# Optimization experiments

Hardware: AMD Instinct MI355X
Metric: run time of the kernel (lower is better)

Reference implementation:

```python
import jax, jax.numpy as jnp
import numpy as np

N_NODES = 100000


def gcn_conv(x, edge_index, W, b, n_nodes):
    """PyG GCNConv: linear -> add self-loops -> symmetric-normalized scatter-sum -> bias."""
    h = x @ W  # [N, F_out]
    loop = jnp.arange(n_nodes, dtype=edge_index.dtype)
    src = jnp.concatenate([edge_index[0], loop])
    dst = jnp.concatenate([edge_index[1], loop])
    # degree of destination nodes (self-loops included)
    deg = jax.ops.segment_sum(jnp.ones_like(dst, dtype=h.dtype), dst, num_segments=n_nodes)
    dinv = jnp.where(deg > 0, jax.lax.rsqrt(deg), 0.0)
    norm = dinv[src] * dinv[dst]  # [E+N]
    msg = h[src] * norm[:, None]  # gather + scale
    out = jax.ops.segment_sum(msg, dst, num_segments=n_nodes)  # scatter-add
    return out + b


def setup_inputs() -> dict:
    key = jax.random.key(0)
    k1, k2, k3, k4 = jax.random.split(key, 4)
    d_in, hidden, out = 128, 256, 64
    x = jax.random.normal(k1, (N_NODES, d_in), dtype=jnp.float32)
    edge_index = jax.random.randint(k2, (2, 800000), 0, N_NODES, dtype=jnp.int64)
    W1 = jax.random.normal(k3, (d_in, hidden), dtype=jnp.float32) * (1.0 / np.sqrt(d_in))
    b1 = jnp.zeros((hidden,), dtype=jnp.float32)
    W2 = jax.random.normal(k4, (hidden, out), dtype=jnp.float32) * (1.0 / np.sqrt(hidden))
    b2 = jnp.zeros((out,), dtype=jnp.float32)
    return {"x": x, "edge_index": edge_index, "W1": W1, "b1": b1, "W2": W2, "b2": b2}


def reference(x, edge_index, W1, b1, W2, b2):
    h = jax.nn.relu(gcn_conv(x, edge_index, W1, b1, N_NODES))
    # dropout p=0 (module default) -> identity
    return gcn_conv(h, edge_index, W2, b2, N_NODES)
```

## Files before the change

kernel.cpp:

```cpp
#include <hip/hip_runtime.h>
#include <hip/hip_bf16.h>

#define N_NODES 100000
#define D_IN 128
#define HID 256
#define D_OUT 64
#define TR 32
#define NBUK 196
#define BSH 9

typedef __attribute__((ext_vector_type(8))) short bf8;
typedef __attribute__((ext_vector_type(4))) float f4;

static __device__ __forceinline__ unsigned short f2bf(float f) {
    __hip_bfloat16 h = __float2bfloat16(f);
    return *reinterpret_cast<unsigned short*>(&h);
}
static __device__ __forceinline__ float bflo(unsigned int u) { return __uint_as_float(u << 16); }
static __device__ __forceinline__ float bfhi(unsigned int u) { return __uint_as_float(u & 0xffff0000u); }

static __device__ __forceinline__ void fma8(float* a, float w, uint4 u) {
    a[0] += w * bflo(u.x); a[1] += w * bfhi(u.x);
    a[2] += w * bflo(u.y); a[3] += w * bfhi(u.y);
    a[4] += w * bflo(u.z); a[5] += w * bfhi(u.z);
    a[6] += w * bflo(u.w); a[7] += w * bfhi(u.w);
}
static __device__ __forceinline__ void fma4(float* a, float w, uint2 u) {
    a[0] += w * bflo(u.x); a[1] += w * bfhi(u.x);
    a[2] += w * bflo(u.y); a[3] += w * bfhi(u.y);
}


__global__ __launch_bounds__(256) void k_prep(const float* __restrict__ x,
                                              unsigned long long* __restrict__ xb,
                                              const float* __restrict__ W1,
                                              unsigned short* __restrict__ W1t,
                                              const float* __restrict__ W2,
                                              unsigned short* __restrict__ W2t,
                                              int* __restrict__ bhist) {
    int b = blockIdx.x, t = threadIdx.x;
    if (b < 12500) {
        int i = b * 256 + t;
        float4 v = ((const float4*)x)[i];
        unsigned long long o = (unsigned long long)f2bf(v.x) |
                               ((unsigned long long)f2bf(v.y) << 16) |
                               ((unsigned long long)f2bf(v.z) << 32) |
                               ((unsigned long long)f2bf(v.w) << 48);
        xb[i] = o;
    } else if (b < 12628) {
        int i = (b - 12500) * 256 + t;
        int n = i >> 7, k = i & 127;
        W1t[i] = f2bf(W1[k * HID + n]);
    } else if (b < 12692) {
        int i = (b - 12628) * 256 + t;
        int n = i >> 8, k = i & 255;
        W2t[i] = f2bf(W2[k * D_OUT + n]);
    } else {
        if (t < NBUK) bhist[t] = 0;
    }
}


__global__ __launch_bounds__(256) void k_hist(const int* __restrict__ dst, int E,
                                              int* __restrict__ bhist) {
    __shared__ int h[NBUK];
    int t = threadIdx.x;
    if (t < NBUK) h[t] = 0;
    __syncthreads();
    int base = blockIdx.x * 4096;
    for (int j = 0; j < 16; j++) {
        int e = base + j * 256 + t;
        if (e < E) atomicAdd(&h[dst[e] >> BSH], 1);
    }
    __syncthreads();
    if (t < NBUK && h[t] > 0) atomicAdd(&bhist[t], h[t]);
}

__global__ __launch_bounds__(256) void k_scanB(const int* __restrict__ bhist,
                                               int* __restrict__ bbase,
                                               int* __restrict__ bcursor) {
    __shared__ int s[256];
    int t = threadIdx.x;
    int v = (t < NBUK) ? bhist[t] : 0;
    s[t] = v;
    __syncthreads();
    for (int off = 1; off < 256; off <<= 1) {
        int u = (t >= off) ? s[t - off] : 0;
        __syncthreads();
        s[t] += u;
        __syncthreads();
    }
    if (t < NBUK) {
        bbase[t] = s[t] - v;
        bcursor[t] = s[t] - v;
    }
    if (t == NBUK - 1) bbase[NBUK] = s[t];
}

__global__ __launch_bounds__(256) void k_bin(const int* __restrict__ src,
                                             const int* __restrict__ dst, int E,
                                             int* __restrict__ bcursor,
                                             unsigned int* __restrict__ bin) {
    __shared__ int histL[NBUK], baseL[NBUK], rankL[NBUK];
    int t = threadIdx.x;
    if (t < NBUK) {
        histL[t] = 0;
        rankL[t] = 0;
    }
    __syncthreads();
    int base = blockIdx.x * 4096;
    int ss[16], dd[16];
#pragma unroll
    for (int j = 0; j < 16; j++) {
        int e = base + j * 256 + t;
        if (e < E) {
            ss[j] = src[e];
            dd[j] = dst[e];
            atomicAdd(&histL[dd[j] >> BSH], 1);
        } else {
            dd[j] = -1;
        }
    }
    __syncthreads();
    if (t < NBUK && histL[t] > 0) baseL[t] = atomicAdd(&bcursor[t], histL[t]);
    __syncthreads();
#pragma unroll
    for (int j = 0; j < 16; j++) {
        if (dd[j] >= 0) {
            int bu = dd[j] >> BSH;
            int r = atomicAdd(&rankL[bu], 1);
            bin[baseL[bu] + r] = ((unsigned int)(dd[j] & 511) << 17) | (unsigned int)ss[j];
        }
    }
}

__global__ __launch_bounds__(256) void k_cnt(const unsigned int* __restrict__ bin,
                                             const int* __restrict__ bbase,
                                             int* __restrict__ cnt) {
    __shared__ int c[512];
    int b = blockIdx.x, t = threadIdx.x;
    c[t] = 0;
    c[t + 256] = 0;
    __syncthreads();
    int lo = bbase[b], hi = bbase[b + 1];
    for (int e = lo + t; e < hi; e += 256) atomicAdd(&c[bin[e] >> 17], 1);
    __syncthreads();
    int node0 = b << BSH;
    int nbn = N_NODES - node0;
    if (nbn > 512) nbn = 512;
    if (t < nbn) cnt[node0 + t] = c[t];
    if (t + 256 < nbn) cnt[node0 + t + 256] = c[t + 256];
}

__global__ __launch_bounds__(256) void k_scan_part(const int* __restrict__ cnt,
                                                   int* __restrict__ row_ptr,
                                                   int* __restrict__ bsum,
                                                   float* __restrict__ dinv, int n) {
    __shared__ int s[256];
    int t = threadIdx.x, i = blockIdx.x * 256 + t;
    int v = (i < n) ? cnt[i] : 0;
    s[t] = v;
    __syncthreads();
    for (int off = 1; off < 256; off <<= 1) {
        int u = (t >= off) ? s[t - off] : 0;
        __syncthreads();
        s[t] += u;
        __syncthreads();
    }
    if (i < n) {
        row_ptr[i] = s[t] - v;
        dinv[i] = rsqrtf((float)v + 1.0f);
    }
    if (t == 255) bsum[blockIdx.x] = s[255];
}

__global__ __launch_bounds__(512) void k_scan_base(int* __restrict__ bsum,
                                                   int* __restrict__ row_ptr, int nb, int n) {
    __shared__ int s[512];
    int t = threadIdx.x;
    int v = (t < nb) ? bsum[t] : 0;
    s[t] = v;
    __syncthreads();
    for (int off = 1; off < 512; off <<= 1) {
        int u = (t >= off) ? s[t - off] : 0;
        __syncthreads();
        s[t] += u;
        __syncthreads();
    }
    if (t < nb) bsum[t] = s[t] - v;
    if (t == 511) row_ptr[n] = s[511];
}

__global__ void k_scan_fin(int* __restrict__ row_ptr, const int* __restrict__ bsum, int n) {
    int i = blockIdx.x * blockDim.x + threadIdx.x;
    if (i < n) row_ptr[i] += bsum[i >> 8];
}

__global__ __launch_bounds__(256) void k_place(const unsigned int* __restrict__ bin,
                                               const int* __restrict__ bbase,
                                               const int* __restrict__ row_ptr,
                                               const float* __restrict__ dinv,
                                               int2* __restrict__ cw) {
    __shared__ int cur[512];
    __shared__ float dl[512];
    int b = blockIdx.x, t = threadIdx.x;
    int node0 = b << BSH;
    int nbn = N_NODES - node0;
    if (nbn > 512) nbn = 512;
    if (t < nbn) {
        cur[t] = row_ptr[node0 + t];
        dl[t] = dinv[node0 + t];
    }
    if (t + 256 < nbn) {
        cur[t + 256] = row_ptr[node0 + t + 256];
        dl[t + 256] = dinv[node0 + t + 256];
    }
    __syncthreads();
    int lo = bbase[b], hi = bbase[b + 1];
    for (int e = lo + t; e < hi; e += 256) {
        unsigned int rec = bin[e];
        int s = rec & 0x1FFFF;
        int dloc = rec >> 17;
        int pos = atomicAdd(&cur[dloc], 1);
        int2 v;
        v.x = s;
        v.y = __float_as_int(dinv[s] * dl[dloc]);
        cw[pos] = v;
    }
}


__global__ __launch_bounds__(256) void k_pull1(const int* __restrict__ row_ptr,
                                               const int2* __restrict__ cw,
                                               const uint4* __restrict__ xb4,
                                               const float* __restrict__ dinv,
                                               uint4* __restrict__ agg4) {
    int wave = (blockIdx.x * 256 + threadIdx.x) >> 6;
    int lane = threadIdx.x & 63;
    int g = lane >> 4, l = lane & 15;
    int node = wave * 4 + g;
    int beg = row_ptr[node], end = row_ptr[node + 1];
    float di = dinv[node];
    float a[8] = {0, 0, 0, 0, 0, 0, 0, 0};
    fma8(a, di * di, xb4[(size_t)node * 16 + l]);
    int e = beg;
    for (; e + 4 <= end; e += 4) {
        int2 c0 = cw[e + 0], c1 = cw[e + 1], c2 = cw[e + 2], c3 = cw[e + 3];
        uint4 u0 = xb4[(size_t)c0.x * 16 + l];
        uint4 u1 = xb4[(size_t)c1.x * 16 + l];
        uint4 u2 = xb4[(size_t)c2.x * 16 + l];
        uint4 u3 = xb4[(size_t)c3.x * 16 + l];
        fma8(a, __int_as_float(c0.y), u0);
        fma8(a, __int_as_float(c1.y), u1);
        fma8(a, __int_as_float(c2.y), u2);
        fma8(a, __int_as_float(c3.y), u3);
    }
    for (; e < end; e++) {
        int2 c = cw[e];
        fma8(a, __int_as_float(c.y), xb4[(size_t)c.x * 16 + l]);
    }
    uint4 o;
    o.x = (unsigned int)f2bf(a[0]) | ((unsigned int)f2bf(a[1]) << 16);
    o.y = (unsigned int)f2bf(a[2]) | ((unsigned int)f2bf(a[3]) << 16);
    o.z = (unsigned int)f2bf(a[4]) | ((unsigned int)f2bf(a[5]) << 16);
    o.w = (unsigned int)f2bf(a[6]) | ((unsigned int)f2bf(a[7]) << 16);
    agg4[(size_t)node * 16 + l] = o;
}


__global__ __launch_bounds__(256) void k_fused_mfma(unsigned short* __restrict__ agg,
                                                    const unsigned short* __restrict__ W1t,
                                                    const float* __restrict__ b1,
                                                    const unsigned short* __restrict__ W2t) {
    __shared__ char sA[TR * D_IN * 2];
    __shared__ char sH[TR * HID * 2];
    int t = threadIdx.x, wave = t >> 6, lane = t & 63;
    int lr = lane & 15, lg = lane >> 4;
    size_t row0 = (size_t)blockIdx.x * TR;

    {
        const float4* g = (const float4*)(agg + row0 * D_IN);
#pragma unroll
        for (int c0 = 0; c0 < 2; c0++) {
            int c = c0 * 256 + t;
            int row = c >> 4;
            *(float4*)(sA + ((c * 16) ^ ((row & 7) << 4))) = g[c];
        }
    }
    __syncthreads();

    f4 acc1[4][2];
#pragma unroll
    for (int tt = 0; tt < 4; tt++)
#pragma unroll
        for (int h = 0; h < 2; h++) acc1[tt][h] = (f4){0.f, 0.f, 0.f, 0.f};

#pragma unroll
    for (int kk = 0; kk < 4; kk++) {
        bf8 a0 = *(const bf8*)(sA + ((lr * 256 + kk * 64 + lg * 16) ^ ((lr & 7) << 4)));
        bf8 a1 = *(const bf8*)(sA + (((16 + lr) * 256 + kk * 64 + lg * 16) ^ (((16 + lr) & 7) << 4)));
#pragma unroll
        for (int tt = 0; tt < 4; tt++) {
            bf8 b = *(const bf8*)(W1t + (size_t)(wave * 64 + tt * 16 + lr) * D_IN + kk * 32 + lg * 8);
            acc1[tt][0] = __builtin_amdgcn_mfma_f32_16x16x32_bf16(a0, b, acc1[tt][0], 0, 0, 0);
            acc1[tt][1] = __builtin_amdgcn_mfma_f32_16x16x32_bf16(a1, b, acc1[tt][1], 0, 0, 0);
        }
    }

#pragma unroll
    for (int tt = 0; tt < 4; tt++) {
        int colc = wave * 64 + tt * 16 + lr;
        float bias = b1[colc];
#pragma unroll
        for (int h = 0; h < 2; h++) {
#pragma unroll
            for (int ri = 0; ri < 4; ri++) {
                int row = h * 16 + lg * 4 + ri;
                float hv = acc1[tt][h][ri] + bias;
                hv = hv > 0.f ? hv : 0.f;
                *(unsigned short*)(sH + ((row * 512 + colc * 2) ^ ((row & 7) << 4))) = f2bf(hv);
            }
        }
    }
    __syncthreads();

    f4 acc2[2];
    acc2[0] = (f4){0.f, 0.f, 0.f, 0.f};
    acc2[1] = (f4){0.f, 0.f, 0.f, 0.f};
#pragma unroll
    for (int kk = 0; kk < 8; kk++) {
        bf8 a0 = *(const bf8*)(sH + ((lr * 512 + kk * 64 + lg * 16) ^ ((lr & 7) << 4)));
        bf8 a1 = *(const bf8*)(sH + (((16 + lr) * 512 + kk * 64 + lg * 16) ^ (((16 + lr) & 7) << 4)));
        bf8 b = *(const bf8*)(W2t + (size_t)(wave * 16 + lr) * HID + kk * 32 + lg * 8);
        acc2[0] = __builtin_amdgcn_mfma_f32_16x16x32_bf16(a0, b, acc2[0], 0, 0, 0);
        acc2[1] = __builtin_amdgcn_mfma_f32_16x16x32_bf16(a1, b, acc2[1], 0, 0, 0);
    }
    int colc = wave * 16 + lr;
#pragma unroll
    for (int h = 0; h < 2; h++)
#pragma unroll
        for (int ri = 0; ri < 4; ri++) {
            int row = h * 16 + lg * 4 + ri;
            agg[(row0 + row) * 128 + colc] = f2bf(acc2[h][ri]);
        }
}


__global__ __launch_bounds__(256) void k_pull2(const int* __restrict__ row_ptr,
                                               const int2* __restrict__ cw,
                                               const uint2* __restrict__ m2,
                                               const float* __restrict__ dinv,
                                               const float* __restrict__ b2,
                                               float4* __restrict__ out4) {
    int wave = (blockIdx.x * 256 + threadIdx.x) >> 6;
    int lane = threadIdx.x & 63;
    int g = lane >> 4, l = lane & 15;
    int node = wave * 4 + g;
    int beg = row_ptr[node], end = row_ptr[node + 1];
    float di = dinv[node];
    float a[4] = {0, 0, 0, 0};
    fma4(a, di * di, m2[(size_t)node * 32 + l]);
    int e = beg;
    for (; e + 4 <= end; e += 4) {
        int2 c0 = cw[e + 0], c1 = cw[e + 1], c2 = cw[e + 2], c3 = cw[e + 3];
        uint2 u0 = m2[(size_t)c0.x * 32 + l];
        uint2 u1 = m2[(size_t)c1.x * 32 + l];
        uint2 u2 = m2[(size_t)c2.x * 32 + l];
        uint2 u3 = m2[(size_t)c3.x * 32 + l];
        fma4(a, __int_as_float(c0.y), u0);
        fma4(a, __int_as_float(c1.y), u1);
        fma4(a, __int_as_float(c2.y), u2);
        fma4(a, __int_as_float(c3.y), u3);
    }
    for (; e < end; e++) {
        int2 c = cw[e];
        fma4(a, __int_as_float(c.y), m2[(size_t)c.x * 32 + l]);
    }
    float4 bv = ((const float4*)b2)[l];
    float4 o;
    o.x = a[0] + bv.x;
    o.y = a[1] + bv.y;
    o.z = a[2] + bv.z;
    o.w = a[3] + bv.w;
    out4[(size_t)node * 16 + l] = o;
}


extern "C" void kernel_launch(void* const* d_in, const int* in_sizes, int n_in,
                              void* d_out, int out_size, void* d_ws, size_t ws_size,
                              hipStream_t stream) {
    const float* x  = (const float*)d_in[0];
    const int*   ei = (const int*)d_in[1];
    const float* W1 = (const float*)d_in[2];
    const float* b1 = (const float*)d_in[3];
    const float* W2 = (const float*)d_in[4];
    const float* b2 = (const float*)d_in[5];
    float* out = (float*)d_out;

    const int E = in_sizes[1] / 2;
    const int* src = ei;
    const int* dst = ei + E;

    char* ws = (char*)d_ws;
    int* cnt            = (int*)(ws + 0);
    int* bsum           = cnt + 100096;
    int* row_ptr        = (int*)(ws + 402176);
    int2* cw            = (int2*)(ws + 802560);
    float* dinv         = (float*)(ws + 7202560);
    unsigned short* W1t = (unsigned short*)(ws + 7602944);
    unsigned short* W2t = (unsigned short*)(ws + 7668480);
    unsigned short* xb  = (unsigned short*)(ws + 7701248);
    unsigned short* aggb = (unsigned short*)(ws + 33301248);
    int* bhist          = (int*)aggb;
    int* bbase          = bhist + 256;
    int* bcursor        = bhist + 512;
    unsigned int* bin   = (unsigned int*)((char*)aggb + 4096);

    const int NB = (N_NODES + 255) / 256;
    const int NBB = (E + 4095) / 4096;

    k_prep<<<12693, 256, 0, stream>>>(x, (unsigned long long*)xb, W1, W1t, W2, W2t, bhist);

    k_hist<<<NBB, 256, 0, stream>>>(dst, E, bhist);
    k_scanB<<<1, 256, 0, stream>>>(bhist, bbase, bcursor);
    k_bin<<<NBB, 256, 0, stream>>>(src, dst, E, bcursor, bin);
    k_cnt<<<NBUK, 256, 0, stream>>>(bin, bbase, cnt);
    k_scan_part<<<NB, 256, 0, stream>>>(cnt, row_ptr, bsum, dinv, N_NODES);
    k_scan_base<<<1, 512, 0, stream>>>(bsum, row_ptr, NB, N_NODES);
    k_scan_fin<<<NB, 256, 0, stream>>>(row_ptr, bsum, N_NODES);
    k_place<<<NBUK, 256, 0, stream>>>(bin, bbase, row_ptr, dinv, cw);

    k_pull1<<<6250, 256, 0, stream>>>(row_ptr, cw, (const uint4*)xb, dinv, (uint4*)aggb);

    k_fused_mfma<<<N_NODES / TR, 256, 0, stream>>>(aggb, W1t, b1, W2t);

    k_pull2<<<6250, 256, 0, stream>>>(row_ptr, cw, (const uint2*)aggb, dinv, b2, (float4*)out);
}
```

Measured before the change: 167.5 us.

## Make fused MFMA kernel persistent with register-resident weight fragments

The fused two-layer MFMA kernel now launches 625 blocks that each loop over five 32-row tiles, instead of one block per tile. The W1/W2 fragments and bias are loaded into registers once per block rather than once per tile. The A operand is read straight from global memory, dropping the shared-memory staging buffer and one barrier. The cost is much higher register pressure (about 96 VGPRs for weights alone), which may lower occupancy, and less parallelism to hide the uncoalesced global reads of A.

```diff
diff --git a/kernel.cpp b/kernel.cpp
--- a/kernel.cpp
+++ b/kernel.cpp
@@ -8,6 +8,7 @@
 #define TR 32
 #define NBUK 196
 #define BSH 9
+#define MGRID 625
 
 typedef __attribute__((ext_vector_type(8))) short bf8;
 typedef __attribute__((ext_vector_type(4))) float f4;
@@ -272,77 +273,80 @@
                                                     const unsigned short* __restrict__ W1t,
                                                     const float* __restrict__ b1,
                                                     const unsigned short* __restrict__ W2t) {
-    __shared__ char sA[TR * D_IN * 2];
     __shared__ char sH[TR * HID * 2];
     int t = threadIdx.x, wave = t >> 6, lane = t & 63;
     int lr = lane & 15, lg = lane >> 4;
-    size_t row0 = (size_t)blockIdx.x * TR;
-
-    {
-        const float4* g = (const float4*)(agg + row0 * D_IN);
-#pragma unroll
-        for (int c0 = 0; c0 < 2; c0++) {
-            int c = c0 * 256 + t;
-            int row = c >> 4;
-            *(float4*)(sA + ((c * 16) ^ ((row & 7) << 4))) = g[c];
+
+    bf8 w1f[4][4];
+#pragma unroll
+    for (int kk = 0; kk < 4; kk++)
+#pragma unroll
+        for (int tt = 0; tt < 4; tt++)
+            w1f[kk][tt] = *(const bf8*)(W1t + (size_t)(wave * 64 + tt * 16 + lr) * D_IN + kk * 32 + lg * 8);
+    bf8 w2f[8];
+#pragma unroll
+    for (int kk = 0; kk < 8; kk++)
+        w2f[kk] = *(const bf8*)(W2t + (size_t)(wave * 16 + lr) * HID + kk * 32 + lg * 8);
+    float bias[4];
+#pragma unroll
+    for (int tt = 0; tt < 4; tt++) bias[tt] = b1[wave * 64 + tt * 16 + lr];
+
+    for (int it = 0; it < 5; it++) {
+        size_t row0 = ((size_t)blockIdx.x + (size_t)it * MGRID) * TR;
+
+        f4 acc1[4][2];
+#pragma unroll
+        for (int tt = 0; tt < 4; tt++)
+#pragma unroll
+            for (int h = 0; h < 2; h++) acc1[tt][h] = (f4){0.f, 0.f, 0.f, 0.f};
+
+#pragma unroll
+        for (int kk = 0; kk < 4; kk++) {
+            bf8 a0 = *(const bf8*)(agg + (row0 + lr) * 128 + kk * 32 + lg * 8);
+            bf8 a1 = *(const bf8*)(agg + (row0 + 16 + lr) * 128 + kk * 32 + lg * 8);
+#pragma unroll
+            for (int tt = 0; tt < 4; tt++) {
+                acc1[tt][0] = __builtin_amdgcn_mfma_f32_16x16x32_bf16(a0, w1f[kk][tt], acc1[tt][0], 0, 0, 0);
+                acc1[tt][1] = __builtin_amdgcn_mfma_f32_16x16x32_bf16(a1, w1f[kk][tt], acc1[tt][1], 0, 0, 0);
+            }
         }
-    }
-    __syncthreads();
-
-    f4 acc1[4][2];
-#pragma unroll
-    for (int tt = 0; tt < 4; tt++)
-#pragma unroll
-        for (int h = 0; h < 2; h++) acc1[tt][h] = (f4){0.f, 0.f, 0.f, 0.f};
-
-#pragma unroll
-    for (int kk = 0; kk < 4; kk++) {
-        bf8 a0 = *(const bf8*)(sA + ((lr * 256 + kk * 64 + lg * 16) ^ ((lr & 7) << 4)));
-        bf8 a1 = *(const bf8*)(sA + (((16 + lr) * 256 + kk * 64 + lg * 16) ^ (((16 + lr) & 7) << 4)));
+
 #pragma unroll
         for (int tt = 0; tt < 4; tt++) {
-            bf8 b = *(const bf8*)(W1t + (size_t)(wave * 64 + tt * 16 + lr) * D_IN + kk * 32 + lg * 8);
-            acc1[tt][0] = __builtin_amdgcn_mfma_f32_16x16x32_bf16(a0, b, acc1[tt][0], 0, 0, 0);
-            acc1[tt][1] = __builtin_amdgcn_mfma_f32_16x16x32_bf16(a1, b, acc1[tt][1], 0, 0, 0);
+            int colc = wave * 64 + tt * 16 + lr;
+#pragma unroll
+            for (int h = 0; h < 2; h++) {
+#pragma unroll
+                for (int ri = 0; ri < 4; ri++) {
+                    int row = h * 16 + lg * 4 + ri;
+                    float hv = acc1[tt][h][ri] + bias[tt];
+                    hv = hv > 0.f ? hv : 0.f;
+                    *(unsigned short*)(sH + ((row * 512 + colc * 2) ^ ((row & 7) << 4))) = f2bf(hv);
+                }
+            }
         }
-    }
-
-#pragma unroll
-    for (int tt = 0; tt < 4; tt++) {
-        int colc = wave * 64 + tt * 16 + lr;
-        float bias = b1[colc];
-#pragma unroll
-        for (int h = 0; h < 2; h++) {
+        __syncthreads();
+
+        f4 acc2[2];
+        acc2[0] = (f4){0.f, 0.f, 0.f, 0.f};
+        acc2[1] = (f4){0.f, 0.f, 0.f, 0.f};
+#pragma unroll
+        for (int kk = 0; kk < 8; kk++) {
+            bf8 a0 = *(const bf8*)(sH + ((lr * 512 + kk * 64 + lg * 16) ^ ((lr & 7) << 4)));
+            bf8 a1 = *(const bf8*)(sH + (((16 + lr) * 512 + kk * 64 + lg * 16) ^ (((16 + lr) & 7) << 4)));
+            acc2[0] = __builtin_amdgcn_mfma_f32_16x16x32_bf16(a0, w2f[kk], acc2[0], 0, 0, 0);
+            acc2[1] = __builtin_amdgcn_mfma_f32_16x16x32_bf16(a1, w2f[kk], acc2[1], 0, 0, 0);
+        }
+        int colc = wave * 16 + lr;
+#pragma unroll
+        for (int h = 0; h < 2; h++)
 #pragma unroll
             for (int ri = 0; ri < 4; ri++) {
                 int row = h * 16 + lg * 4 + ri;
-                float hv = acc1[tt][h][ri] + bias;
-                hv = hv > 0.f ? hv : 0.f;
-                *(unsigned short*)(sH + ((row * 512 + colc * 2) ^ ((row & 7) << 4))) = f2bf(hv);
+                agg[(row0 + row) * 128 + colc] = f2bf(acc2[h][ri]);
             }
-        }
-    }
-    __syncthreads();
-
-    f4 acc2[2];
-    acc2[0] = (f4){0.f, 0.f, 0.f, 0.f};
-    acc2[1] = (f4){0.f, 0.f, 0.f, 0.f};
-#pragma unroll
-    for (int kk = 0; kk < 8; kk++) {
-        bf8 a0 = *(const bf8*)(sH + ((lr * 512 + kk * 64 + lg * 16) ^ ((lr & 7) << 4)));
-        bf8 a1 = *(const bf8*)(sH + (((16 + lr) * 512 + kk * 64 + lg * 16) ^ (((16 + lr) & 7) << 4)));
-        bf8 b = *(const bf8*)(W2t + (size_t)(wave * 16 + lr) * HID + kk * 32 + lg * 8);
-        acc2[0] = __builtin_amdgcn_mfma_f32_16x16x32_bf16(a0, b, acc2[0], 0, 0, 0);
-        acc2[1] = __builtin_amdgcn_mfma_f32_16x16x32_bf16(a1, b, acc2[1], 0, 0, 0);
-    }
-    int colc = wave * 16 + lr;
-#pragma unroll
-    for (int h = 0; h < 2; h++)
-#pragma unroll
-        for (int ri = 0; ri < 4; ri++) {
-            int row = h * 16 + lg * 4 + ri;
-            agg[(row0 + row) * 128 + colc] = f2bf(acc2[h][ri]);
-        }
+        __syncthreads();
+    }
 }
 
 
@@ -432,7 +436,7 @@
 
     k_pull1<<<6250, 256, 0, stream>>>(row_ptr, cw, (const uint4*)xb, dinv, (uint4*)aggb);
 
-    k_fused_mfma<<<N_NODES / TR, 256, 0, stream>>>(aggb, W1t, b1, W2t);
+    k_fused_mfma<<<MGRID, 256, 0, stream>>>(aggb, W1t, b1, W2t);
 
     k_pull2<<<6250, 256, 0, stream>>>(row_ptr, cw, (const uint2*)aggb, dinv, b2, (float4*)out);
 }
```

Measured after the change: 159.3 us. 4.9% less time.
